# Performance work log

Measured on AMD Instinct MI355X. Metric: run time of the kernel, lower is better.

The kernel has to match this reference:

```python
import jax, jax.numpy as jnp
import numpy as np

B, S, ENC_D, DEC_D, ATTN_D, OUT_D = 32, 2048, 1024, 1024, 1024, 1024
SCALING = 1.0


def setup_inputs() -> dict:
    key = jax.random.key(0)
    ks = jax.random.split(key, 10)
    enc_states = jax.random.normal(ks[0], (B, S, ENC_D), dtype=jnp.float32)
    # lengths in [S//2, S] so every row has at least one valid position
    enc_len = jax.random.randint(ks[1], (B,), S // 2, S + 1, dtype=jnp.int32)
    dec_states = jax.random.normal(ks[2], (B, DEC_D), dtype=jnp.float32)
    s = 0.02
    W_enc = jax.random.normal(ks[3], (ENC_D, ATTN_D), dtype=jnp.float32) * s
    b_enc = jnp.zeros((ATTN_D,), dtype=jnp.float32)
    W_dec = jax.random.normal(ks[4], (DEC_D, ATTN_D), dtype=jnp.float32) * s
    b_dec = jnp.zeros((ATTN_D,), dtype=jnp.float32)
    w_attn = jax.random.normal(ks[5], (ATTN_D,), dtype=jnp.float32) * s
    W_out = jax.random.normal(ks[6], (ENC_D, OUT_D), dtype=jnp.float32) * s
    b_out = jnp.zeros((OUT_D,), dtype=jnp.float32)
    return {
        "enc_states": enc_states,
        "dec_states": dec_states,
        "W_enc": W_enc, "b_enc": b_enc,
        "W_dec": W_dec, "b_dec": b_dec,
        "w_attn": w_attn,
        "W_out": W_out, "b_out": b_out,
        "enc_len": enc_len,
    }


def reference(enc_states, dec_states, W_enc, b_enc, W_dec, b_dec, w_attn, W_out, b_out, enc_len):
    # precomputed_enc_h = mlp_enc(enc_states): [B, S, ATTN_D]
    enc_h = jnp.einsum("bse,ea->bsa", enc_states, W_enc) + b_enc
    # dec_h = mlp_dec(dec_states): [B, ATTN_D]
    dec_h = dec_states @ W_dec + b_dec
    # additive (Bahdanau) score: tanh(enc_h + dec_h) . w_attn -> [B, S]
    attn = jnp.einsum("bsa,a->bs", jnp.tanh(enc_h + dec_h[:, None, :]), w_attn)
    # length mask
    mask = jnp.arange(enc_states.shape[1])[None, :] < enc_len[:, None]  # [B, S]
    attn = jnp.where(mask, attn, -jnp.inf)
    attn = jax.nn.softmax(attn * SCALING, axis=-1)
    # context = attn @ enc_states -> [B, ENC_D]
    context = jnp.einsum("bs,bse->be", attn, enc_states)
    context = context @ W_out + b_out
    return (context, attn)
```

## Files before the change

kernel.cpp:

```cpp
#include <hip/hip_runtime.h>
#include <cstdint>
#include <cstddef>

#define BATCH 32
#define SEQ   2048
#define DIM   1024
#define MROWS (BATCH*SEQ)

typedef __attribute__((ext_vector_type(4))) float  floatx4;
typedef __attribute__((ext_vector_type(8))) short  short8;

__device__ __forceinline__ unsigned short f2bf(float f) {
  unsigned int u = __float_as_uint(f);
  u += 0x7fffu + ((u >> 16) & 1u);
  return (unsigned short)(u >> 16);
}

__device__ __forceinline__ void async16(const void* g, void* l) {
  __builtin_amdgcn_global_load_lds(
      (const __attribute__((address_space(1))) unsigned int*)g,
      (__attribute__((address_space(3))) unsigned int*)l, 16, 0, 0);
}

__device__ __forceinline__ float fast_tanh(float x) {
  float e = __expf(2.0f * x);
  return 1.0f - 2.0f * __builtin_amdgcn_rcpf(1.0f + e);
}

__global__ void k_convert(const float* __restrict__ enc, const int* __restrict__ enc_len,
                          unsigned short* __restrict__ Abf) {
  int b = blockIdx.y;
  int r0 = blockIdx.x * 8;
  if (r0 >= enc_len[b]) return;
  size_t base = ((size_t)b * SEQ + r0) * DIM;
  const float4* src = (const float4*)(enc + base);
  ushort4* dst = (ushort4*)(Abf + base);
  int tid = threadIdx.x;
#pragma unroll
  for (int i = 0; i < 8; ++i) {
    float4 v = src[tid + i * 256];
    ushort4 h;
    h.x = f2bf(v.x); h.y = f2bf(v.y); h.z = f2bf(v.z); h.w = f2bf(v.w);
    dst[tid + i * 256] = h;
  }
}

__global__ void k_transpose(const float* __restrict__ W, unsigned short* __restrict__ Wt) {
  __shared__ float tile[32][33];
  int n0 = blockIdx.x * 32, k0 = blockIdx.y * 32;
  int tx = threadIdx.x, ty = threadIdx.y;
#pragma unroll
  for (int i = 0; i < 4; ++i) {
    int y = ty + i * 8;
    tile[y][tx] = W[(size_t)(k0 + y) * DIM + n0 + tx];
  }
  __syncthreads();
#pragma unroll
  for (int i = 0; i < 4; ++i) {
    int y = ty + i * 8;
    Wt[(size_t)(n0 + y) * DIM + k0 + tx] = f2bf(tile[tx][y]);
  }
}

__global__ void k_dech(const float* __restrict__ dec, const float* __restrict__ W_dec,
                       const float* __restrict__ b_dec, const float* __restrict__ b_enc,
                       float* __restrict__ dech) {
  int b = blockIdx.y, z = blockIdx.z;
  int a = blockIdx.x * 256 + threadIdx.x;
  float acc = (z == 0) ? (b_dec[a] + b_enc[a]) : 0.0f;
  const float* dr = dec + (size_t)b * DIM + z * 128;
  const float* wc = W_dec + (size_t)z * 128 * DIM + a;
#pragma unroll 8
  for (int e = 0; e < 128; ++e)
    acc = fmaf(dr[e], wc[(size_t)e * DIM], acc);
  atomicAdd(&dech[(size_t)b * DIM + a], acc);
}

__global__ void __launch_bounds__(256, 2) k_gemm_bf16(
    const unsigned short* __restrict__ Abf,
    const unsigned short* __restrict__ Wt,
    const float* __restrict__ dech,
    const float* __restrict__ w_attn,
    const int* __restrict__ enc_len,
    float* __restrict__ score)
{
  int linear = blockIdx.x;
  int xcd = linear & 7;
  int j   = linear >> 3;
  int rb  = xcd * 64 + (j >> 3);
  int nb  = j & 7;

  int bb  = rb >> 4;
  int len = enc_len[bb];
  if (((rb & 15) * 128) >= len) return;

  __shared__ __align__(16) unsigned short sA[128 * 32];
  __shared__ __align__(16) unsigned short sB[128 * 32];

  int tid  = threadIdx.x;
  int w    = tid >> 6, lane = tid & 63;
  int wm   = (w >> 1) * 64, wn = (w & 1) * 64;
  int li   = lane & 15, g = lane >> 4;

  const unsigned short* Ab = Abf + (size_t)rb * 128 * DIM;
  const unsigned short* Bb = Wt  + (size_t)nb * 128 * DIM;

  floatx4 acc[4][4] = {};

  for (int kb = 0; kb < 32; ++kb) {
    __syncthreads();
#pragma unroll
    for (int r = 0; r < 2; ++r) {
      int seg = r * 4 + w;
      int p   = seg * 64 + lane;
      int row = p >> 2, q = p & 3;
      size_t goff = (size_t)row * DIM + kb * 32 + q * 8;
      async16(Ab + goff, (char*)sA + seg * 1024);
      async16(Bb + goff, (char*)sB + seg * 1024);
    }
    __syncthreads();

    short8 af[4], bfr[4];
#pragma unroll
    for (int t = 0; t < 4; ++t) {
      int row = wm + t * 16 + li;
      af[t]  = *(const short8*)&sA[(row * 4 + g) * 8];
      int n  = wn + t * 16 + li;
      bfr[t] = *(const short8*)&sB[(n * 4 + g) * 8];
    }
#pragma unroll
    for (int tm = 0; tm < 4; ++tm)
#pragma unroll
      for (int tn = 0; tn < 4; ++tn)
        acc[tm][tn] = __builtin_amdgcn_mfma_f32_16x16x32_bf16(af[tm], bfr[tn], acc[tm][tn], 0, 0, 0);
  }

  float dh[4], wa[4];
#pragma unroll
  for (int tn = 0; tn < 4; ++tn) {
    int n = nb * 128 + wn + tn * 16 + li;
    dh[tn] = dech[(size_t)bb * DIM + n];
    wa[tn] = w_attn[n];
  }
#pragma unroll
  for (int tm = 0; tm < 4; ++tm) {
    int mrow = rb * 128 + wm + tm * 16 + g * 4;
#pragma unroll
    for (int r = 0; r < 4; ++r) {
      float v = 0.0f;
#pragma unroll
      for (int tn = 0; tn < 4; ++tn)
        v = fmaf(wa[tn], fast_tanh(acc[tm][tn][r] + dh[tn]), v);
      v += __shfl_xor(v, 1);
      v += __shfl_xor(v, 2);
      v += __shfl_xor(v, 4);
      v += __shfl_xor(v, 8);
      if (li == 0) atomicAdd(&score[mrow + r], v);
    }
  }
}

__global__ void __launch_bounds__(256, 2) k_gemm_f32(
    const float* __restrict__ A, const unsigned short* __restrict__ Wt,
    const float* __restrict__ dech, const float* __restrict__ w_attn,
    const int* __restrict__ enc_len, float* __restrict__ score)
{
  int linear = blockIdx.x;
  int xcd = linear & 7;
  int j   = linear >> 3;
  int rb  = xcd * 64 + (j >> 3);
  int nb  = j & 7;
  int bb  = rb >> 4;
  int len = enc_len[bb];
  if (((rb & 15) * 128) >= len) return;

  __shared__ __align__(16) unsigned short sA[128 * 40];
  __shared__ __align__(16) unsigned short sB[128 * 32];

  int tid  = threadIdx.x;
  int w    = tid >> 6, lane = tid & 63;
  int wm   = (w >> 1) * 64, wn = (w & 1) * 64;
  int li   = lane & 15, g = lane >> 4;

  const float*          Abase = A  + (size_t)rb * 128 * DIM;
  const unsigned short* Bbase = Wt + (size_t)nb * 128 * DIM;

  floatx4 acc[4][4] = {};

  for (int kb = 0; kb < 32; ++kb) {
    __syncthreads();
#pragma unroll
    for (int i = 0; i < 2; ++i) {
      int c  = (w * 2 + i) * 64 + lane;
      int n  = c >> 2;
      int kh = (c & 3) ^ ((n >> 1) & 3);
      async16(Bbase + (size_t)n * DIM + kb * 32 + kh * 8, (char*)sB + (w * 2 + i) * 1024);
    }
#pragma unroll
    for (int i = 0; i < 4; ++i) {
      int f4  = tid + i * 256;
      int row = f4 >> 3, kq = f4 & 7;
      float4 v = *(const float4*)(Abase + (size_t)row * DIM + kb * 32 + kq * 4);
      ushort4 h;
      h.x = f2bf(v.x); h.y = f2bf(v.y); h.z = f2bf(v.z); h.w = f2bf(v.w);
      *(ushort4*)&sA[row * 40 + kq * 4] = h;
    }
    __syncthreads();

    short8 af[4], bfr[4];
#pragma unroll
    for (int t = 0; t < 4; ++t) {
      int row = wm + t * 16 + li;
      af[t] = *(const short8*)&sA[row * 40 + g * 8];
      int nl = wn + t * 16 + li;
      int phys = (nl << 2) | (g ^ ((nl >> 1) & 3));
      bfr[t] = *(const short8*)((const char*)sB + phys * 16);
    }
#pragma unroll
    for (int tm = 0; tm < 4; ++tm)
#pragma unroll
      for (int tn = 0; tn < 4; ++tn)
        acc[tm][tn] = __builtin_amdgcn_mfma_f32_16x16x32_bf16(af[tm], bfr[tn], acc[tm][tn], 0, 0, 0);
  }

  float dh[4], wa[4];
#pragma unroll
  for (int tn = 0; tn < 4; ++tn) {
    int n = nb * 128 + wn + tn * 16 + li;
    dh[tn] = dech[(size_t)bb * DIM + n];
    wa[tn] = w_attn[n];
  }
#pragma unroll
  for (int tm = 0; tm < 4; ++tm) {
    int mrow = rb * 128 + wm + tm * 16 + g * 4;
#pragma unroll
    for (int r = 0; r < 4; ++r) {
      float v = 0.0f;
#pragma unroll
      for (int tn = 0; tn < 4; ++tn)
        v = fmaf(wa[tn], fast_tanh(acc[tm][tn][r] + dh[tn]), v);
      v += __shfl_xor(v, 1);
      v += __shfl_xor(v, 2);
      v += __shfl_xor(v, 4);
      v += __shfl_xor(v, 8);
      if (li == 0) atomicAdd(&score[mrow + r], v);
    }
  }
}

__global__ void k_softmax(const float* __restrict__ score, const int* __restrict__ enc_len,
                          float* __restrict__ attn) {
  int b = blockIdx.x, tid = threadIdx.x;
  int len = enc_len[b];
  __shared__ float red[256];
  float v[8];
  float m = -1e30f;
#pragma unroll
  for (int i = 0; i < 8; ++i) {
    int s = tid + i * 256;
    v[i] = score[(size_t)b * SEQ + s];
    if (s < len) m = fmaxf(m, v[i]);
  }
  red[tid] = m; __syncthreads();
  for (int st = 128; st > 0; st >>= 1) {
    if (tid < st) red[tid] = fmaxf(red[tid], red[tid + st]);
    __syncthreads();
  }
  float mx = red[0]; __syncthreads();
  float sum = 0.0f;
#pragma unroll
  for (int i = 0; i < 8; ++i) {
    int s = tid + i * 256;
    float e = (s < len) ? __expf(v[i] - mx) : 0.0f;
    v[i] = e; sum += e;
  }
  red[tid] = sum; __syncthreads();
  for (int st = 128; st > 0; st >>= 1) {
    if (tid < st) red[tid] += red[tid + st];
    __syncthreads();
  }
  float inv = 1.0f / red[0];
#pragma unroll
  for (int i = 0; i < 8; ++i)
    attn[(size_t)b * SEQ + tid + i * 256] = v[i] * inv;
}

__global__ void k_context(const float* __restrict__ enc, const float* __restrict__ attn,
                          const int* __restrict__ enc_len, float* __restrict__ ctx) {
  int b = blockIdx.y, sc = blockIdx.x;
  int len = enc_len[b];
  int s0 = sc * 32;
  if (s0 >= len) return;
  int cnt = min(32, len - s0);
  int tid = threadIdx.x;
  const float* base = enc + ((size_t)b * SEQ + s0) * DIM + tid * 4;
  const float* ap   = attn + (size_t)b * SEQ + s0;
  float a0 = 0.f, a1 = 0.f, a2 = 0.f, a3 = 0.f;
  int i = 0;
  for (; i + 8 <= cnt; i += 8) {
    float4 x[8];
    float  w[8];
#pragma unroll
    for (int u = 0; u < 8; ++u)
      x[u] = *(const float4*)(base + (size_t)(i + u) * DIM);
#pragma unroll
    for (int u = 0; u < 8; ++u)
      w[u] = ap[i + u];
#pragma unroll
    for (int u = 0; u < 8; ++u) {
      a0 = fmaf(w[u], x[u].x, a0); a1 = fmaf(w[u], x[u].y, a1);
      a2 = fmaf(w[u], x[u].z, a2); a3 = fmaf(w[u], x[u].w, a3);
    }
  }
  for (; i < cnt; ++i) {
    float w = ap[i];
    float4 x = *(const float4*)(base + (size_t)i * DIM);
    a0 = fmaf(w, x.x, a0); a1 = fmaf(w, x.y, a1);
    a2 = fmaf(w, x.z, a2); a3 = fmaf(w, x.w, a3);
  }
  float* c = ctx + (size_t)b * DIM + tid * 4;
  atomicAdd(c + 0, a0); atomicAdd(c + 1, a1);
  atomicAdd(c + 2, a2); atomicAdd(c + 3, a3);
}

__global__ void k_out(const float* __restrict__ ctx, const float* __restrict__ W_out,
                      const float* __restrict__ b_out, float* __restrict__ out) {
  int b = blockIdx.y, z = blockIdx.z;
  int o = blockIdx.x * 256 + threadIdx.x;
  float acc = (z == 0) ? b_out[o] : 0.0f;
  const float* cr = ctx + (size_t)b * DIM + z * 128;
  const float* wc = W_out + (size_t)z * 128 * DIM + o;
#pragma unroll 8
  for (int e = 0; e < 128; ++e)
    acc = fmaf(cr[e], wc[(size_t)e * DIM], acc);
  atomicAdd(&out[(size_t)b * DIM + o], acc);
}

extern "C" void kernel_launch(void* const* d_in, const int* in_sizes, int n_in,
                              void* d_out, int out_size, void* d_ws, size_t ws_size,
                              hipStream_t stream) {
  (void)in_sizes; (void)n_in; (void)out_size;
  const float* enc_states = (const float*)d_in[0];
  const float* dec_states = (const float*)d_in[1];
  const float* W_enc      = (const float*)d_in[2];
  const float* b_enc      = (const float*)d_in[3];
  const float* W_dec      = (const float*)d_in[4];
  const float* b_dec      = (const float*)d_in[5];
  const float* w_attn     = (const float*)d_in[6];
  const float* W_out      = (const float*)d_in[7];
  const float* b_out      = (const float*)d_in[8];
  const int*   enc_len    = (const int*)  d_in[9];

  float* out_ctx  = (float*)d_out;
  float* out_attn = (float*)d_out + BATCH * DIM;

  char* ws = (char*)d_ws;
  unsigned short* Wt  = (unsigned short*)ws;
  float* score = (float*)(ws + (2u << 20));
  float* ctx   = (float*)(ws + (2u << 20) + 262144);
  float* dech  = (float*)(ws + (2u << 20) + 262144 + 131072);
  unsigned short* Abf = (unsigned short*)(ws + (3u << 20));
  const bool fast = ws_size >= ((size_t)(3u << 20) + ((size_t)MROWS * DIM * 2));

  hipMemsetAsync(ws + (2u << 20), 0, 262144 + 131072 + 131072, stream);
  hipMemsetAsync(d_out, 0, (size_t)BATCH * DIM * sizeof(float), stream);

  k_transpose<<<dim3(32, 32), dim3(32, 8), 0, stream>>>(W_enc, Wt);
  k_dech<<<dim3(4, BATCH, 8), 256, 0, stream>>>(dec_states, W_dec, b_dec, b_enc, dech);
  if (fast) {
    k_convert<<<dim3(SEQ / 8, BATCH), 256, 0, stream>>>(enc_states, enc_len, Abf);
    k_gemm_bf16<<<4096, 256, 0, stream>>>(Abf, Wt, dech, w_attn, enc_len, score);
  } else {
    k_gemm_f32<<<4096, 256, 0, stream>>>(enc_states, Wt, dech, w_attn, enc_len, score);
  }
  k_softmax<<<BATCH, 256, 0, stream>>>(score, enc_len, out_attn);
  k_context<<<dim3(64, BATCH), 256, 0, stream>>>(enc_states, out_attn, enc_len, ctx);
  k_out<<<dim3(4, BATCH, 8), 256, 0, stream>>>(ctx, W_out, b_out, out_ctx);
}
```

Measured before the change: 612.1 us.

## Replace bf16 score GEMM with 256x256-tile double-buffered pipelined kernel

Replaces the 128x128, 256-thread score GEMM with a 256x256-tile, 512-thread kernel. It double-buffers 64-wide K slices in 128KB of LDS using an XOR-swizzled layout, and interleaves async global-to-LDS loads with MFMA quarter-steps, separated by explicit barriers, sched_barrier, setprio and vmcnt waits. The larger tiles raise data reuse and the overlap hides load latency. In exchange, LDS use rises sharply, which can limit occupancy, and masked-length skipping now works at coarser 256-row granularity, so more padded work may be computed.

```diff
diff --git a/kernel.cpp b/kernel.cpp
--- a/kernel.cpp
+++ b/kernel.cpp
@@ -76,7 +76,13 @@
   atomicAdd(&dech[(size_t)b * DIM + a], acc);
 }
 
-__global__ void __launch_bounds__(256, 2) k_gemm_bf16(
+#define PH_BAR do { asm volatile("" ::: "memory"); __builtin_amdgcn_s_barrier(); asm volatile("" ::: "memory"); } while(0)
+#define SCHED0 __builtin_amdgcn_sched_barrier(0)
+#define SP1 __builtin_amdgcn_s_setprio(1)
+#define SP0 __builtin_amdgcn_s_setprio(0)
+#define VMCNT(n) asm volatile("s_waitcnt vmcnt(" #n ")" ::: "memory")
+
+__global__ void __launch_bounds__(512, 2) k_gemm256(
     const unsigned short* __restrict__ Abf,
     const unsigned short* __restrict__ Wt,
     const float* __restrict__ dech,
@@ -84,67 +90,122 @@
     const int* __restrict__ enc_len,
     float* __restrict__ score)
 {
-  int linear = blockIdx.x;
-  int xcd = linear & 7;
-  int j   = linear >> 3;
-  int rb  = xcd * 64 + (j >> 3);
-  int nb  = j & 7;
-
-  int bb  = rb >> 4;
+  int bid = blockIdx.x;
+  int t  = (bid & 7) * 128 + (bid >> 3);
+  int nb = t & 3;
+  int rt = t >> 2;
+  int bb = rt >> 3;
   int len = enc_len[bb];
-  if (((rb & 15) * 128) >= len) return;
-
-  __shared__ __align__(16) unsigned short sA[128 * 32];
-  __shared__ __align__(16) unsigned short sB[128 * 32];
-
-  int tid  = threadIdx.x;
-  int w    = tid >> 6, lane = tid & 63;
-  int wm   = (w >> 1) * 64, wn = (w & 1) * 64;
-  int li   = lane & 15, g = lane >> 4;
-
-  const unsigned short* Ab = Abf + (size_t)rb * 128 * DIM;
-  const unsigned short* Bb = Wt  + (size_t)nb * 128 * DIM;
-
-  floatx4 acc[4][4] = {};
-
-  for (int kb = 0; kb < 32; ++kb) {
-    __syncthreads();
-#pragma unroll
-    for (int r = 0; r < 2; ++r) {
-      int seg = r * 4 + w;
-      int p   = seg * 64 + lane;
-      int row = p >> 2, q = p & 3;
-      size_t goff = (size_t)row * DIM + kb * 32 + q * 8;
-      async16(Ab + goff, (char*)sA + seg * 1024);
-      async16(Bb + goff, (char*)sB + seg * 1024);
-    }
-    __syncthreads();
-
-    short8 af[4], bfr[4];
-#pragma unroll
-    for (int t = 0; t < 4; ++t) {
-      int row = wm + t * 16 + li;
-      af[t]  = *(const short8*)&sA[(row * 4 + g) * 8];
-      int n  = wn + t * 16 + li;
-      bfr[t] = *(const short8*)&sB[(n * 4 + g) * 8];
-    }
-#pragma unroll
-    for (int tm = 0; tm < 4; ++tm)
-#pragma unroll
-      for (int tn = 0; tn < 4; ++tn)
-        acc[tm][tn] = __builtin_amdgcn_mfma_f32_16x16x32_bf16(af[tm], bfr[tn], acc[tm][tn], 0, 0, 0);
-  }
+  if (((rt & 7) * 256) >= len) return;
+
+  __shared__ __align__(16) char lds[131072];
+
+  int tid = threadIdx.x;
+  int w = tid >> 6, lane = tid & 63;
+  int wr = w >> 2;
+  int wc = w & 3;
+  int li = lane & 15, g = lane >> 4;
+  int xl = (li & 7) << 4;
+
+  const char* Ag = (const char*)(Abf + (size_t)rt * 256 * DIM);
+  const char* Bg = (const char*)(Wt  + (size_t)nb * 256 * DIM);
+
+  size_t soff[2][2];
+  int    ldso[2][2];
+#pragma unroll
+  for (int h = 0; h < 2; ++h)
+#pragma unroll
+    for (int i = 0; i < 2; ++i) {
+      int P = h * 16384 + (w * 2 + i) * 1024 + lane * 16;
+      int L = P ^ (((P >> 7) & 7) << 4);
+      soff[h][i] = (size_t)(L >> 7) * (DIM * 2) + (L & 127);
+      ldso[h][i] = h * 16384 + (w * 2 + i) * 1024;
+    }
+
+#define STAGE_A(buf, h, kt) do { \
+  async16(Ag + soff[h][0] + (size_t)(kt) * 128, lds + (buf) * 32768 + ldso[h][0]); \
+  async16(Ag + soff[h][1] + (size_t)(kt) * 128, lds + (buf) * 32768 + ldso[h][1]); \
+} while (0)
+#define STAGE_B(buf, h, kt) do { \
+  async16(Bg + soff[h][0] + (size_t)(kt) * 128, lds + 65536 + (buf) * 32768 + ldso[h][0]); \
+  async16(Bg + soff[h][1] + (size_t)(kt) * 128, lds + 65536 + (buf) * 32768 + ldso[h][1]); \
+} while (0)
+
+  short8 aF[4][2];
+  short8 bF[2][2][2];
+  floatx4 acc[8][4] = {};
+
+#define READ_A(buf, mh) do { \
+  const char* base_ = lds + (buf) * 32768 + (wr * 128 + (mh) * 64 + li) * 128; \
+  int c0_ = (g * 16) ^ xl; \
+  _Pragma("unroll") for (int tmq = 0; tmq < 4; ++tmq) { \
+    aF[tmq][0] = *(const short8*)(base_ + tmq * 2048 + c0_); \
+    aF[tmq][1] = *(const short8*)(base_ + tmq * 2048 + (c0_ ^ 64)); \
+  } \
+} while (0)
+#define READ_B(buf, nh) do { \
+  const char* base_ = lds + 65536 + (buf) * 32768 + (wc * 64 + (nh) * 32 + li) * 128; \
+  int c0_ = (g * 16) ^ xl; \
+  _Pragma("unroll") for (int tnq = 0; tnq < 2; ++tnq) { \
+    bF[nh][tnq][0] = *(const short8*)(base_ + tnq * 2048 + c0_); \
+    bF[nh][tnq][1] = *(const short8*)(base_ + tnq * 2048 + (c0_ ^ 64)); \
+  } \
+} while (0)
+#define MFMA_Q(mh, nh) do { \
+  _Pragma("unroll") for (int ks = 0; ks < 2; ++ks) \
+  _Pragma("unroll") for (int tmq = 0; tmq < 4; ++tmq) \
+  _Pragma("unroll") for (int tnq = 0; tnq < 2; ++tnq) \
+    acc[(mh) * 4 + tmq][(nh) * 2 + tnq] = __builtin_amdgcn_mfma_f32_16x16x32_bf16( \
+        aF[tmq][ks], bF[nh][tnq][ks], acc[(mh) * 4 + tmq][(nh) * 2 + tnq], 0, 0, 0); \
+} while (0)
+
+#define TILE_STEP(CUR, KTN, KTN2, MODE) do { \
+   \
+  READ_A(CUR, 0); \
+  READ_B(CUR, 0); \
+  if ((MODE) < 2) STAGE_A((CUR) ^ 1, 1, KTN); \
+  PH_BAR; SCHED0; SP1; MFMA_Q(0, 0); SP0; SCHED0; \
+  PH_BAR; \
+   \
+  READ_B(CUR, 1); \
+  if ((MODE) < 2) STAGE_B((CUR) ^ 1, 0, KTN); \
+  PH_BAR; SCHED0; SP1; MFMA_Q(0, 1); SP0; SCHED0; \
+  PH_BAR; \
+   \
+  READ_A(CUR, 1); \
+  if ((MODE) < 2) STAGE_B((CUR) ^ 1, 1, KTN); \
+  PH_BAR; SCHED0; SP1; MFMA_Q(1, 1); SP0; SCHED0; \
+  PH_BAR; \
+   \
+  if ((MODE) == 0) STAGE_A(CUR, 0, KTN2); \
+  PH_BAR; SCHED0; SP1; MFMA_Q(1, 0); SP0; SCHED0; \
+  if ((MODE) == 0) { VMCNT(2); } else if ((MODE) == 1) { VMCNT(0); } \
+  PH_BAR; \
+} while (0)
+
+  STAGE_A(0, 0, 0); STAGE_A(0, 1, 0); STAGE_B(0, 0, 0); STAGE_B(0, 1, 0);
+  STAGE_A(1, 0, 1);
+  VMCNT(2);
+  PH_BAR;
+
+#pragma unroll 1
+  for (int u = 0; u < 14; u += 2) {
+    TILE_STEP(0, u + 1, u + 2, 0);
+    TILE_STEP(1, u + 2, u + 3, 0);
+  }
+  TILE_STEP(0, 15, 0, 1);
+  TILE_STEP(1, 0, 0, 2);
 
   float dh[4], wa[4];
 #pragma unroll
   for (int tn = 0; tn < 4; ++tn) {
-    int n = nb * 128 + wn + tn * 16 + li;
+    int n = nb * 256 + wc * 64 + tn * 16 + li;
     dh[tn] = dech[(size_t)bb * DIM + n];
     wa[tn] = w_attn[n];
   }
 #pragma unroll
-  for (int tm = 0; tm < 4; ++tm) {
-    int mrow = rb * 128 + wm + tm * 16 + g * 4;
+  for (int tm = 0; tm < 8; ++tm) {
+    int mrow = rt * 256 + wr * 128 + tm * 16 + g * 4;
 #pragma unroll
     for (int r = 0; r < 4; ++r) {
       float v = 0.0f;
@@ -158,6 +219,12 @@
       if (li == 0) atomicAdd(&score[mrow + r], v);
     }
   }
+#undef TILE_STEP
+#undef MFMA_Q
+#undef READ_B
+#undef READ_A
+#undef STAGE_B
+#undef STAGE_A
 }
 
 __global__ void __launch_bounds__(256, 2) k_gemm_f32(
@@ -369,7 +436,7 @@
   k_dech<<<dim3(4, BATCH, 8), 256, 0, stream>>>(dec_states, W_dec, b_dec, b_enc, dech);
   if (fast) {
     k_convert<<<dim3(SEQ / 8, BATCH), 256, 0, stream>>>(enc_states, enc_len, Abf);
-    k_gemm_bf16<<<4096, 256, 0, stream>>>(Abf, Wt, dech, w_attn, enc_len, score);
+    k_gemm256<<<1024, 512, 0, stream>>>(Abf, Wt, dech, w_attn, enc_len, score);
   } else {
     k_gemm_f32<<<4096, 256, 0, stream>>>(enc_states, Wt, dech, w_attn, enc_len, score);
   }
```

Measured after the change: 601.5 us. No clear change (-1.7%).
